# Kernel optimization log

Hardware: AMD Instinct MI355X
Metric: run time of the kernel (lower is better)

## Reference

```python
import jax, jax.numpy as jnp
import numpy as np

NEG_INF = -9e15
ALPHA = 0.2  # LeakyReLU negative slope

N = 4096
NFEAT = 512
NHID = 256
NEMBED = 128
NHEADS = 4
OUT1 = NHID // NHEADS   # 64
OUT2 = NEMBED // NHEADS # 32


def _gat_layer(x, adj_mask, W, a):
    # x: [N, F_in]; adj_mask: [N, N] bool; W: [H, F_in, F_out]; a: [H, 2*F_out]
    Fo = W.shape[-1]
    Wh = jnp.einsum('nf,hfo->hno', x, W)                     # [H, N, Fo]
    a_src = jnp.einsum('hno,ho->hn', Wh, a[:, :Fo])          # [H, N]
    a_dst = jnp.einsum('hno,ho->hn', Wh, a[:, Fo:])          # [H, N]
    e = a_src[:, :, None] + a_dst[:, None, :]                # [H, N, N]
    e = jax.nn.leaky_relu(e, negative_slope=ALPHA)
    e = jnp.where(adj_mask[None, :, :], e, NEG_INF)
    att = jax.nn.softmax(e, axis=-1)                         # [H, N, N]
    h = jnp.einsum('hnm,hmo->hno', att, Wh)                  # [H, N, Fo]
    h = jax.nn.elu(h)                                        # concat=True -> ELU
    # concat heads: [N, H*Fo]
    return jnp.transpose(h, (1, 0, 2)).reshape(x.shape[0], -1)


def setup_inputs() -> dict:
    key = jax.random.key(0)
    k1, k2, k3, k4, k5, k6 = jax.random.split(key, 6)
    x = jax.random.normal(k1, (N, NFEAT), dtype=jnp.float32)
    adj = (jax.random.uniform(k2, (N, N)) < 0.01).astype(jnp.float32)
    # per-head GAT params, xavier-uniform-like init (stacked over heads)
    def xavier(k, shape, fan):
        bound = np.sqrt(6.0 / fan)
        return jax.random.uniform(k, shape, minval=-bound, maxval=bound, dtype=jnp.float32)
    W1 = xavier(k3, (NHEADS, NFEAT, OUT1), NFEAT + OUT1)
    a1 = xavier(k4, (NHEADS, 2 * OUT1), 2 * OUT1 + 1)
    W2 = xavier(k5, (NHEADS, NHID, OUT2), NHID + OUT2)
    a2 = xavier(k6, (NHEADS, 2 * OUT2), 2 * OUT2 + 1)
    return {'x': x, 'adj': adj, 'W1': W1, 'a1': a1, 'W2': W2, 'a2': a2}


def reference(x, adj, W1, a1, W2, a2):
    # eval mode: dropout is identity
    adj_mask = adj > 0
    h1 = _gat_layer(x, adj_mask, W1, a1)    # [N, NHID]
    h2 = _gat_layer(h1, adj_mask, W2, a2)   # [N, NEMBED]
    return h2
```

## Files before the change

### kernel.cpp

```cpp
#include <hip/hip_runtime.h>
#include <hip/hip_bf16.h>
#include <cstdint>
#include <cstddef>

#define NNODES 4096
#define NHEADS 4
#define NBR_STRIDE 128

typedef __attribute__((ext_vector_type(8))) short bf16x8v;
typedef __attribute__((ext_vector_type(4))) float f32x4;

__device__ inline unsigned short bf16_rn(float f) {
    unsigned int u = __float_as_uint(f);
    u += 0x7FFFu + ((u >> 16) & 1u);
    return (unsigned short)(u >> 16);
}
__device__ inline float bf16_f32(unsigned short s) {
    return __uint_as_float(((unsigned int)s) << 16);
}

__global__ __launch_bounds__(256) void build_nbr_kernel(
    const float* __restrict__ adj, int* __restrict__ nbr, int* __restrict__ deg) {
    int wave = threadIdx.x >> 6;
    int lane = threadIdx.x & 63;
    int row = blockIdx.x * 4 + wave;
    const float4* arow = reinterpret_cast<const float4*>(adj + (size_t)row * NNODES);
    float4 v[16];
    #pragma unroll
    for (int it = 0; it < 16; ++it) v[it] = arow[it * 64 + lane];
    unsigned long long lt = (1ull << lane) - 1ull;
    int base = 0;
    #pragma unroll
    for (int it = 0; it < 16; ++it) {
        bool b0 = v[it].x > 0.f, b1 = v[it].y > 0.f, b2 = v[it].z > 0.f, b3 = v[it].w > 0.f;
        unsigned long long m0 = __ballot(b0);
        unsigned long long m1 = __ballot(b1);
        unsigned long long m2 = __ballot(b2);
        unsigned long long m3 = __ballot(b3);
        int pre = __popcll(m0 & lt) + __popcll(m1 & lt) +
                  __popcll(m2 & lt) + __popcll(m3 & lt);
        int pos = base + pre;
        int colb = it * 256 + lane * 4;
        if (b0) { if (pos < NBR_STRIDE) nbr[row * NBR_STRIDE + pos] = colb;     pos++; }
        if (b1) { if (pos < NBR_STRIDE) nbr[row * NBR_STRIDE + pos] = colb + 1; pos++; }
        if (b2) { if (pos < NBR_STRIDE) nbr[row * NBR_STRIDE + pos] = colb + 2; pos++; }
        if (b3) { if (pos < NBR_STRIDE) nbr[row * NBR_STRIDE + pos] = colb + 3; pos++; }
        base += __popcll(m0) + __popcll(m1) + __popcll(m2) + __popcll(m3);
    }
    if (lane == 0) deg[row] = base < NBR_STRIDE ? base : NBR_STRIDE;
}

__global__ __launch_bounds__(256) void pack_b_both_kernel(
    const float* __restrict__ W1, const float* __restrict__ W2,
    unsigned short* __restrict__ B1h, unsigned short* __restrict__ B1l,
    unsigned short* __restrict__ B2h, unsigned short* __restrict__ B2l) {
    int t = blockIdx.x * 256 + threadIdx.x;
    if (t < 256 * 512) {
        int n = t >> 9, k = t & 511;
        int h = n >> 6, o = n & 63;
        float v = W1[((size_t)h * 512 + k) * 64 + o];
        unsigned short hi = bf16_rn(v);
        B1h[t] = hi;
        B1l[t] = bf16_rn(v - bf16_f32(hi));
    } else {
        int u = t - 256 * 512;
        if (u < 128 * 256) {
            int n = u >> 8, k = u & 255;
            int h = n >> 5, o = n & 31;
            float v = W2[((size_t)h * 256 + k) * 32 + o];
            unsigned short hi = bf16_rn(v);
            B2h[u] = hi;
            B2l[u] = bf16_rn(v - bf16_f32(hi));
        }
    }
}

template <int K, int N, int FO>
__global__ __launch_bounds__(256) void gemm_split_kernel(
    const float* __restrict__ A,
    const unsigned short* __restrict__ Bh, const unsigned short* __restrict__ Bl,
    const float* __restrict__ a, float* __restrict__ C,
    float* __restrict__ asrc, float* __restrict__ adst) {
    constexpr int BM = 32, BN = 64, BK = 64, LP = BK + 8;
    __shared__ unsigned short Alh[BM][LP], All[BM][LP];
    __shared__ unsigned short Blh[BN][LP], Bll[BN][LP];
    __shared__ float reds[2][BM], redd[2][BM];
    int tid = threadIdx.x;
    int wave = tid >> 6, lane = tid & 63;
    int rowBase = blockIdx.x * BM;
    int colBase = blockIdx.y * BN;
    int wr = wave >> 1, wc = wave & 1;
    int lr = lane & 15, lk = lane >> 4;
    f32x4 acc0 = {0.f, 0.f, 0.f, 0.f};
    f32x4 acc1 = {0.f, 0.f, 0.f, 0.f};
    int ar = tid >> 3;
    int ac = (tid & 7) * 8;
    for (int k0 = 0; k0 < K; k0 += BK) {
        float4 a0 = *reinterpret_cast<const float4*>(&A[(size_t)(rowBase + ar) * K + k0 + ac]);
        float4 a1 = *reinterpret_cast<const float4*>(&A[(size_t)(rowBase + ar) * K + k0 + ac + 4]);
        uint4 bh0 = *reinterpret_cast<const uint4*>(&Bh[(size_t)(colBase + ar) * K + k0 + ac]);
        uint4 bl0 = *reinterpret_cast<const uint4*>(&Bl[(size_t)(colBase + ar) * K + k0 + ac]);
        uint4 bh1 = *reinterpret_cast<const uint4*>(&Bh[(size_t)(colBase + 32 + ar) * K + k0 + ac]);
        uint4 bl1 = *reinterpret_cast<const uint4*>(&Bl[(size_t)(colBase + 32 + ar) * K + k0 + ac]);
        __syncthreads();
        ushort4 h4, l4;
        h4.x = bf16_rn(a0.x); l4.x = bf16_rn(a0.x - bf16_f32(h4.x));
        h4.y = bf16_rn(a0.y); l4.y = bf16_rn(a0.y - bf16_f32(h4.y));
        h4.z = bf16_rn(a0.z); l4.z = bf16_rn(a0.z - bf16_f32(h4.z));
        h4.w = bf16_rn(a0.w); l4.w = bf16_rn(a0.w - bf16_f32(h4.w));
        *reinterpret_cast<ushort4*>(&Alh[ar][ac]) = h4;
        *reinterpret_cast<ushort4*>(&All[ar][ac]) = l4;
        h4.x = bf16_rn(a1.x); l4.x = bf16_rn(a1.x - bf16_f32(h4.x));
        h4.y = bf16_rn(a1.y); l4.y = bf16_rn(a1.y - bf16_f32(h4.y));
        h4.z = bf16_rn(a1.z); l4.z = bf16_rn(a1.z - bf16_f32(h4.z));
        h4.w = bf16_rn(a1.w); l4.w = bf16_rn(a1.w - bf16_f32(h4.w));
        *reinterpret_cast<ushort4*>(&Alh[ar][ac + 4]) = h4;
        *reinterpret_cast<ushort4*>(&All[ar][ac + 4]) = l4;
        *reinterpret_cast<uint4*>(&Blh[ar][ac]) = bh0;
        *reinterpret_cast<uint4*>(&Bll[ar][ac]) = bl0;
        *reinterpret_cast<uint4*>(&Blh[32 + ar][ac]) = bh1;
        *reinterpret_cast<uint4*>(&Bll[32 + ar][ac]) = bl1;
        __syncthreads();
        #pragma unroll
        for (int ks = 0; ks < 2; ++ks) {
            int kb = ks * 32 + lk * 8;
            bf16x8v ah = *reinterpret_cast<const bf16x8v*>(&Alh[wr * 16 + lr][kb]);
            bf16x8v al = *reinterpret_cast<const bf16x8v*>(&All[wr * 16 + lr][kb]);
            bf16x8v b0h = *reinterpret_cast<const bf16x8v*>(&Blh[wc * 32 + lr][kb]);
            bf16x8v b0l = *reinterpret_cast<const bf16x8v*>(&Bll[wc * 32 + lr][kb]);
            bf16x8v b1h = *reinterpret_cast<const bf16x8v*>(&Blh[wc * 32 + 16 + lr][kb]);
            bf16x8v b1l = *reinterpret_cast<const bf16x8v*>(&Bll[wc * 32 + 16 + lr][kb]);
            acc0 = __builtin_amdgcn_mfma_f32_16x16x32_bf16(ah, b0h, acc0, 0, 0, 0);
            acc0 = __builtin_amdgcn_mfma_f32_16x16x32_bf16(ah, b0l, acc0, 0, 0, 0);
            acc0 = __builtin_amdgcn_mfma_f32_16x16x32_bf16(al, b0h, acc0, 0, 0, 0);
            acc1 = __builtin_amdgcn_mfma_f32_16x16x32_bf16(ah, b1h, acc1, 0, 0, 0);
            acc1 = __builtin_amdgcn_mfma_f32_16x16x32_bf16(ah, b1l, acc1, 0, 0, 0);
            acc1 = __builtin_amdgcn_mfma_f32_16x16x32_bf16(al, b1h, acc1, 0, 0, 0);
        }
    }
    int crow = rowBase + wr * 16 + lk * 4;
    int ccol = colBase + wc * 32 + lr;
    #pragma unroll
    for (int r = 0; r < 4; ++r) {
        C[(size_t)(crow + r) * N + ccol]      = acc0[r];
        C[(size_t)(crow + r) * N + ccol + 16] = acc1[r];
    }
    int n0 = colBase + wc * 32 + lr;
    int hh = n0 / FO;
    int o0 = n0 % FO;
    int o1 = o0 + 16;
    const float* av = a + hh * 2 * FO;
    float aS0 = av[o0], aS1 = av[o1];
    float aD0 = av[FO + o0], aD1 = av[FO + o1];
    float sv[4], dv[4];
    #pragma unroll
    for (int r = 0; r < 4; ++r) {
        sv[r] = acc0[r] * aS0 + acc1[r] * aS1;
        dv[r] = acc0[r] * aD0 + acc1[r] * aD1;
        #pragma unroll
        for (int msk = 1; msk < 16; msk <<= 1) {
            sv[r] += __shfl_xor(sv[r], msk);
            dv[r] += __shfl_xor(dv[r], msk);
        }
    }
    if constexpr (FO == 64) {
        if (lr == 0) {
            #pragma unroll
            for (int r = 0; r < 4; ++r) {
                reds[wc][wr * 16 + lk * 4 + r] = sv[r];
                redd[wc][wr * 16 + lk * 4 + r] = dv[r];
            }
        }
        __syncthreads();
        if (tid < BM) {
            int row = tid;
            asrc[blockIdx.y * NNODES + rowBase + row] = reds[0][row] + reds[1][row];
            adst[blockIdx.y * NNODES + rowBase + row] = redd[0][row] + redd[1][row];
        }
    } else {
        if (lr == 0) {
            #pragma unroll
            for (int r = 0; r < 4; ++r) {
                asrc[hh * NNODES + rowBase + wr * 16 + lk * 4 + r] = sv[r];
                adst[hh * NNODES + rowBase + wr * 16 + lk * 4 + r] = dv[r];
            }
        }
    }
}

template <int FO>
__global__ __launch_bounds__(256) void agg_kernel(
    const float* __restrict__ Wh,
    const float* __restrict__ asrc, const float* __restrict__ adst,
    const int* __restrict__ nbr, const int* __restrict__ deg,
    float* __restrict__ out) {
    __shared__ float2 sw[4][NBR_STRIDE];
    int wslot = threadIdx.x >> 6;
    int lane = threadIdx.x & 63;
    int wid = blockIdx.x * 4 + wslot;
    int n = wid >> 2, h = wid & 3;
    int dg = deg[n];
    const int* lst = nbr + n * NBR_STRIDE;
    float my_as = asrc[h * NNODES + n];

    int c0 = 0, c1 = 0;
    float e0 = -1e30f, e1 = -1e30f;
    if (lane < dg) {
        c0 = lst[lane];
        float e = my_as + adst[h * NNODES + c0];
        e0 = e >= 0.f ? e : 0.2f * e;
    }
    if (lane + 64 < dg) {
        c1 = lst[lane + 64];
        float e = my_as + adst[h * NNODES + c1];
        e1 = e >= 0.f ? e : 0.2f * e;
    }
    float m = fmaxf(e0, e1);
    #pragma unroll
    for (int s = 32; s; s >>= 1) m = fmaxf(m, __shfl_xor(m, s));
    float p0 = (lane < dg) ? __expf(e0 - m) : 0.f;
    float p1 = (lane + 64 < dg) ? __expf(e1 - m) : 0.f;
    float denom = p0 + p1;
    #pragma unroll
    for (int s = 32; s; s >>= 1) denom += __shfl_xor(denom, s);
    float inv = 1.0f / denom;

    if (lane < dg)      sw[wslot][lane]      = make_float2(p0 * inv, __int_as_float(c0));
    if (lane + 64 < dg) sw[wslot][lane + 64] = make_float2(p1 * inv, __int_as_float(c1));
    __syncthreads();

    constexpr int STRIDE = NHEADS * FO;
    constexpr int LPR = FO / 4;
    constexpr int NPS = 64 / LPR;
    int sub = lane / LPR;
    int dim4 = (lane % LPR) * 4;
    const float* whp = Wh + h * FO + dim4;
    f32x4 acc = {0.f, 0.f, 0.f, 0.f};
    int main_n = (dg / (4 * NPS)) * (4 * NPS);
    int k = 0;
    for (; k < main_n; k += 4 * NPS) {
        #pragma unroll
        for (int u = 0; u < 4; ++u) {
            float2 w = sw[wslot][k + u * NPS + sub];
            int col = __float_as_int(w.y);
            float4 v = *reinterpret_cast<const float4*>(&whp[(size_t)col * STRIDE]);
            acc[0] += w.x * v.x;
            acc[1] += w.x * v.y;
            acc[2] += w.x * v.z;
            acc[3] += w.x * v.w;
        }
    }
    for (; k < dg; k += NPS) {
        if (k + sub < dg) {
            float2 w = sw[wslot][k + sub];
            int col = __float_as_int(w.y);
            float4 v = *reinterpret_cast<const float4*>(&whp[(size_t)col * STRIDE]);
            acc[0] += w.x * v.x;
            acc[1] += w.x * v.y;
            acc[2] += w.x * v.z;
            acc[3] += w.x * v.w;
        }
    }
    #pragma unroll
    for (int s = LPR; s < 64; s <<= 1) {
        acc[0] += __shfl_xor(acc[0], s);
        acc[1] += __shfl_xor(acc[1], s);
        acc[2] += __shfl_xor(acc[2], s);
        acc[3] += __shfl_xor(acc[3], s);
    }
    if (lane < LPR) {
        float4 r;
        r.x = acc[0] > 0.f ? acc[0] : expm1f(acc[0]);
        r.y = acc[1] > 0.f ? acc[1] : expm1f(acc[1]);
        r.z = acc[2] > 0.f ? acc[2] : expm1f(acc[2]);
        r.w = acc[3] > 0.f ? acc[3] : expm1f(acc[3]);
        *reinterpret_cast<float4*>(&out[(size_t)n * STRIDE + h * FO + dim4]) = r;
    }
}

extern "C" void kernel_launch(void* const* d_in, const int* in_sizes, int n_in,
                              void* d_out, int out_size, void* d_ws, size_t ws_size,
                              hipStream_t stream) {
    const float* x   = (const float*)d_in[0];
    const float* adj = (const float*)d_in[1];
    const float* W1  = (const float*)d_in[2];
    const float* a1  = (const float*)d_in[3];
    const float* W2  = (const float*)d_in[4];
    const float* a2  = (const float*)d_in[5];
    float* out = (float*)d_out;

    char* p = (char*)d_ws;
    auto alloc = [&](size_t bytes) -> void* {
        void* r = (void*)p;
        p += (bytes + 255) & ~(size_t)255;
        return r;
    };
    int*   nbr = (int*)alloc((size_t)NNODES * NBR_STRIDE * 4);
    int*   deg = (int*)alloc((size_t)NNODES * 4);
    unsigned short* B1h = (unsigned short*)alloc((size_t)256 * 512 * 2);
    unsigned short* B1l = (unsigned short*)alloc((size_t)256 * 512 * 2);
    unsigned short* B2h = (unsigned short*)alloc((size_t)128 * 256 * 2);
    unsigned short* B2l = (unsigned short*)alloc((size_t)128 * 256 * 2);
    float* Wh1 = (float*)alloc((size_t)NNODES * 256 * 4);
    float* as1 = (float*)alloc((size_t)NHEADS * NNODES * 4);
    float* ad1 = (float*)alloc((size_t)NHEADS * NNODES * 4);
    float* h1  = (float*)alloc((size_t)NNODES * 256 * 4);
    float* Wh2 = (float*)alloc((size_t)NNODES * 128 * 4);
    float* as2 = (float*)alloc((size_t)NHEADS * NNODES * 4);
    float* ad2 = (float*)alloc((size_t)NHEADS * NNODES * 4);

    pack_b_both_kernel<<<dim3((256 * 512 + 128 * 256) / 256), dim3(256), 0, stream>>>(
        W1, W2, B1h, B1l, B2h, B2l);
    build_nbr_kernel<<<dim3(NNODES / 4), dim3(256), 0, stream>>>(adj, nbr, deg);

    gemm_split_kernel<512, 256, 64><<<dim3(NNODES / 32, 4), dim3(256), 0, stream>>>(
        x, B1h, B1l, a1, Wh1, as1, ad1);
    agg_kernel<64><<<dim3(NNODES * NHEADS / 4), dim3(256), 0, stream>>>(
        Wh1, as1, ad1, nbr, deg, h1);

    gemm_split_kernel<256, 128, 32><<<dim3(NNODES / 32, 2), dim3(256), 0, stream>>>(
        h1, B2h, B2l, a2, Wh2, as2, ad2);
    agg_kernel<32><<<dim3(NNODES * NHEADS / 4), dim3(256), 0, stream>>>(
        Wh2, as2, ad2, nbr, deg, out);
}
```

Measured before the change: 69.70 us.

## Fuse neighbor-list build with layer-1 GEMM and remap aggregation waves to heads

Merges the adjacency-to-neighbor-list kernel and the first split-bf16 GEMM into one launch, with block index deciding which body runs, so the memory-bound adjacency scan can overlap the compute-bound GEMM and one launch is saved. The aggregation kernel now maps one node per block with one head per wave, drops an unneeded block barrier (each wave only reads its own shared slot), and unrolls the neighbor gather loop by 8 instead of 4. GEMM shared memory moves into a manually carved arena so both bodies can share one kernel. The larger unroll may raise register use and send more work to the tail loop for low-degree nodes.

```diff
diff --git a/kernel.cpp b/kernel.cpp
--- a/kernel.cpp
+++ b/kernel.cpp
@@ -19,11 +19,12 @@
     return __uint_as_float(((unsigned int)s) << 16);
 }
 
-__global__ __launch_bounds__(256) void build_nbr_kernel(
-    const float* __restrict__ adj, int* __restrict__ nbr, int* __restrict__ deg) {
+__device__ inline void build_nbr_body(
+    const float* __restrict__ adj, int* __restrict__ nbr, int* __restrict__ deg,
+    int rowblk) {
     int wave = threadIdx.x >> 6;
     int lane = threadIdx.x & 63;
-    int row = blockIdx.x * 4 + wave;
+    int row = rowblk * 4 + wave;
     const float4* arow = reinterpret_cast<const float4*>(adj + (size_t)row * NNODES);
     float4 v[16];
     #pragma unroll
@@ -76,19 +77,25 @@
 }
 
 template <int K, int N, int FO>
-__global__ __launch_bounds__(256) void gemm_split_kernel(
+__device__ inline void gemm_body(
+    char* arena,
     const float* __restrict__ A,
     const unsigned short* __restrict__ Bh, const unsigned short* __restrict__ Bl,
     const float* __restrict__ a, float* __restrict__ C,
-    float* __restrict__ asrc, float* __restrict__ adst) {
+    float* __restrict__ asrc, float* __restrict__ adst,
+    int bx, int by) {
     constexpr int BM = 32, BN = 64, BK = 64, LP = BK + 8;
-    __shared__ unsigned short Alh[BM][LP], All[BM][LP];
-    __shared__ unsigned short Blh[BN][LP], Bll[BN][LP];
-    __shared__ float reds[2][BM], redd[2][BM];
+    typedef unsigned short (*lds_t)[LP];
+    lds_t Alh = (lds_t)(arena);
+    lds_t All = (lds_t)(arena + 4608);
+    lds_t Blh = (lds_t)(arena + 9216);
+    lds_t Bll = (lds_t)(arena + 18432);
+    float* reds = (float*)(arena + 27648);
+    float* redd = (float*)(arena + 27904);
     int tid = threadIdx.x;
     int wave = tid >> 6, lane = tid & 63;
-    int rowBase = blockIdx.x * BM;
-    int colBase = blockIdx.y * BN;
+    int rowBase = bx * BM;
+    int colBase = by * BN;
     int wr = wave >> 1, wc = wave & 1;
     int lr = lane & 15, lk = lane >> 4;
     f32x4 acc0 = {0.f, 0.f, 0.f, 0.f};
@@ -167,15 +174,15 @@
         if (lr == 0) {
             #pragma unroll
             for (int r = 0; r < 4; ++r) {
-                reds[wc][wr * 16 + lk * 4 + r] = sv[r];
-                redd[wc][wr * 16 + lk * 4 + r] = dv[r];
+                reds[wc * 32 + wr * 16 + lk * 4 + r] = sv[r];
+                redd[wc * 32 + wr * 16 + lk * 4 + r] = dv[r];
             }
         }
         __syncthreads();
         if (tid < BM) {
             int row = tid;
-            asrc[blockIdx.y * NNODES + rowBase + row] = reds[0][row] + reds[1][row];
-            adst[blockIdx.y * NNODES + rowBase + row] = redd[0][row] + redd[1][row];
+            asrc[by * NNODES + rowBase + row] = reds[row] + reds[32 + row];
+            adst[by * NNODES + rowBase + row] = redd[row] + redd[32 + row];
         }
     } else {
         if (lr == 0) {
@@ -186,6 +193,32 @@
             }
         }
     }
+}
+
+__global__ __launch_bounds__(256) void fused1_kernel(
+    const float* __restrict__ adj, int* __restrict__ nbr, int* __restrict__ deg,
+    const float* __restrict__ x,
+    const unsigned short* __restrict__ B1h, const unsigned short* __restrict__ B1l,
+    const float* __restrict__ a1, float* __restrict__ Wh1,
+    float* __restrict__ as1, float* __restrict__ ad1) {
+    __shared__ __align__(16) char arena[28160];
+    int b = blockIdx.x;
+    if (b < 512) {
+        gemm_body<512, 256, 64>(arena, x, B1h, B1l, a1, Wh1, as1, ad1,
+                                b & 127, b >> 7);
+    } else {
+        build_nbr_body(adj, nbr, deg, b - 512);
+    }
+}
+
+template <int K, int N, int FO>
+__global__ __launch_bounds__(256) void gemm_split_kernel(
+    const float* __restrict__ A,
+    const unsigned short* __restrict__ Bh, const unsigned short* __restrict__ Bl,
+    const float* __restrict__ a, float* __restrict__ C,
+    float* __restrict__ asrc, float* __restrict__ adst) {
+    __shared__ __align__(16) char arena[28160];
+    gemm_body<K, N, FO>(arena, A, Bh, Bl, a, C, asrc, adst, blockIdx.x, blockIdx.y);
 }
 
 template <int FO>
@@ -197,8 +230,8 @@
     __shared__ float2 sw[4][NBR_STRIDE];
     int wslot = threadIdx.x >> 6;
     int lane = threadIdx.x & 63;
-    int wid = blockIdx.x * 4 + wslot;
-    int n = wid >> 2, h = wid & 3;
+    int n = blockIdx.x;
+    int h = wslot;
     int dg = deg[n];
     const int* lst = nbr + n * NBR_STRIDE;
     float my_as = asrc[h * NNODES + n];
@@ -227,7 +260,6 @@
 
     if (lane < dg)      sw[wslot][lane]      = make_float2(p0 * inv, __int_as_float(c0));
     if (lane + 64 < dg) sw[wslot][lane + 64] = make_float2(p1 * inv, __int_as_float(c1));
-    __syncthreads();
 
     constexpr int STRIDE = NHEADS * FO;
     constexpr int LPR = FO / 4;
@@ -236,11 +268,11 @@
     int dim4 = (lane % LPR) * 4;
     const float* whp = Wh + h * FO + dim4;
     f32x4 acc = {0.f, 0.f, 0.f, 0.f};
-    int main_n = (dg / (4 * NPS)) * (4 * NPS);
+    int main_n = (dg / (8 * NPS)) * (8 * NPS);
     int k = 0;
-    for (; k < main_n; k += 4 * NPS) {
+    for (; k < main_n; k += 8 * NPS) {
         #pragma unroll
-        for (int u = 0; u < 4; ++u) {
+        for (int u = 0; u < 8; ++u) {
             float2 w = sw[wslot][k + u * NPS + sub];
             int col = __float_as_int(w.y);
             float4 v = *reinterpret_cast<const float4*>(&whp[(size_t)col * STRIDE]);
@@ -287,7 +319,7 @@
     const float* a1  = (const float*)d_in[3];
     const float* W2  = (const float*)d_in[4];
     const float* a2  = (const float*)d_in[5];
-    float* out = (float*)d_out;
+    float* outp = (float*)d_out;
 
     char* p = (char*)d_ws;
     auto alloc = [&](size_t bytes) -> void* {
@@ -311,15 +343,12 @@
 
     pack_b_both_kernel<<<dim3((256 * 512 + 128 * 256) / 256), dim3(256), 0, stream>>>(
         W1, W2, B1h, B1l, B2h, B2l);
-    build_nbr_kernel<<<dim3(NNODES / 4), dim3(256), 0, stream>>>(adj, nbr, deg);
-
-    gemm_split_kernel<512, 256, 64><<<dim3(NNODES / 32, 4), dim3(256), 0, stream>>>(
-        x, B1h, B1l, a1, Wh1, as1, ad1);
-    agg_kernel<64><<<dim3(NNODES * NHEADS / 4), dim3(256), 0, stream>>>(
+    fused1_kernel<<<dim3(512 + NNODES / 4), dim3(256), 0, stream>>>(
+        adj, nbr, deg, x, B1h, B1l, a1, Wh1, as1, ad1);
+    agg_kernel<64><<<dim3(NNODES), dim3(256), 0, stream>>>(
         Wh1, as1, ad1, nbr, deg, h1);
-
     gemm_split_kernel<256, 128, 32><<<dim3(NNODES / 32, 2), dim3(256), 0, stream>>>(
         h1, B2h, B2l, a2, Wh2, as2, ad2);
-    agg_kernel<32><<<dim3(NNODES * NHEADS / 4), dim3(256), 0, stream>>>(
-        Wh2, as2, ad2, nbr, deg, out);
-}
+    agg_kernel<32><<<dim3(NNODES), dim3(256), 0, stream>>>(
+        Wh2, as2, ad2, nbr, deg, outp);
+}
```

After: 66.88 us. -4.0%, faster.
